# Kernel optimization log

Measured on AMD Instinct MI355X. Metric: run time of the kernel, lower is better.

Reference implementation:

```python
import jax, jax.numpy as jnp
import numpy as np

EPS = 1e-10

def setup_inputs() -> dict:
    key = jax.random.key(0)
    k1, k2, k3 = jax.random.split(key, 3)
    B, K, M, X, Y = 64, 4, 3, 256, 256
    predictions = jax.random.uniform(k1, (B, K, X, Y), dtype=jnp.float32)
    inputs = jax.random.normal(k2, (B, M, X, Y), dtype=jnp.float32)
    heart = jax.random.randint(k3, (B, 1, X, Y), 0, 2, dtype=jnp.int32)
    return {"predictions": predictions, "inputs": inputs, "heart": heart}

def reference(predictions, inputs, heart):
    B, K, X, Y = predictions.shape
    M = inputs.shape[1]
    P = X * Y
    pred = predictions.reshape(B, K, P)            # [B,K,P]
    inp = inputs.reshape(B, M, P)                  # [B,M,P]
    w = (heart.reshape(B, P) == 1).astype(pred.dtype)  # ROI mask [B,P]
    pw = pred * w[:, None, :]                      # masked responsibilities [B,K,P]
    s = pw.sum(-1) + EPS                           # [B,K]
    # weighted means/vars over masked pixels
    mu = jnp.einsum('bkp,bmp->bkm', pw, inp) / s[..., None]        # [B,K,M]
    diff = inp[:, None, :, :] - mu[..., None]                      # [B,K,M,P]
    var = jnp.einsum('bkmp,bkp->bkm', diff * diff, pw) / s[..., None] + EPS
    # per-channel Gaussian pdf, product over channels M
    pdf = jnp.exp(-diff * diff / (2.0 * var[..., None])) / jnp.sqrt(2.0 * jnp.pi * var)[..., None]
    temp = jnp.prod(pdf, axis=2)                   # [B,K,P]
    mix = jnp.sum(pred * temp, axis=1)             # [B,P]
    ll = jnp.log(mix + EPS)
    n = w.sum(-1)                                   # pixels in ROI per sample
    loss_b = -(ll * w).sum(-1) / n                 # mean over masked pixels
    return jnp.mean(loss_b)
```

## Files before the change

### kernel.cpp

```cpp
#include <hip/hip_runtime.h>

#define EPS 1e-10f

constexpr int B_ = 64, K_ = 4, M_ = 3, P_ = 65536;
constexpr int THREADS = 256;
constexpr int CHUNK = 2048;
constexpr int BLOCKS_PER_B = P_ / CHUNK;
constexpr int VPT = CHUNK / 4 / THREADS;
constexpr int WAVE_ITERS = CHUNK / 4 / 64;
constexpr int NACC = 29;

__global__ __launch_bounds__(THREADS, 4) void gmm_pass1(
    const float* __restrict__ pred, const float* __restrict__ inp,
    const int* __restrict__ heart, float* __restrict__ sums)
{
    const int blk   = blockIdx.x;
    const int b     = blk / BLOCKS_PER_B;
    const int chunk = blk % BLOCKS_PER_B;
    const int tid   = threadIdx.x;
    const int wv    = tid >> 6;
    const int lane  = tid & 63;

    const float4* pkb = (const float4*)(pred + ((size_t)b * K_ + wv) * P_);
    const float4* ib  = (const float4*)(inp  + (size_t)b * M_ * P_);
    const int4*   hb  = (const int4*)(heart + (size_t)b * P_);
    const int vbase = chunk * (CHUNK / 4);

    float s = 0.f, n = 0.f;
    float t0 = 0.f, t1 = 0.f, t2 = 0.f;
    float u0 = 0.f, u1 = 0.f, u2 = 0.f;

    int v = vbase + lane;
    float4 p_c  = pkb[v];
    float4 x0_c = ib[0 * (P_ / 4) + v];
    float4 x1_c = ib[1 * (P_ / 4) + v];
    float4 x2_c = ib[2 * (P_ / 4) + v];
    int4   h_c  = hb[v];

    #pragma unroll
    for (int it = 0; it < WAVE_ITERS; ++it) {
        float4 p_n, x0_n, x1_n, x2_n; int4 h_n;
        if (it + 1 < WAVE_ITERS) {
            const int vn = vbase + (it + 1) * 64 + lane;
            p_n  = pkb[vn];
            x0_n = ib[0 * (P_ / 4) + vn];
            x1_n = ib[1 * (P_ / 4) + vn];
            x2_n = ib[2 * (P_ / 4) + vn];
            h_n  = hb[vn];
        }

        #define PIX1(C) do {                                                  \
            const float w  = (h_c.C == 1) ? 1.f : 0.f;                        \
            const float pw = p_c.C * w;                                       \
            n += w; s += pw;                                                  \
            t0 = fmaf(pw, x0_c.C, t0);                                        \
            u0 = fmaf(pw * x0_c.C, x0_c.C, u0);                               \
            t1 = fmaf(pw, x1_c.C, t1);                                        \
            u1 = fmaf(pw * x1_c.C, x1_c.C, u1);                               \
            t2 = fmaf(pw, x2_c.C, t2);                                        \
            u2 = fmaf(pw * x2_c.C, x2_c.C, u2);                               \
        } while (0)
        PIX1(x); PIX1(y); PIX1(z); PIX1(w);
        #undef PIX1

        if (it + 1 < WAVE_ITERS) {
            p_c = p_n; x0_c = x0_n; x1_c = x1_n; x2_c = x2_n; h_c = h_n;
        }
    }

    float vals[8] = { s, t0, t1, t2, u0, u1, u2, n };
    __shared__ float lds[4 * 8];
    #pragma unroll
    for (int j = 0; j < 8; ++j) {
        float x = vals[j];
        #pragma unroll
        for (int off = 32; off; off >>= 1) x += __shfl_down(x, off);
        vals[j] = x;
    }
    if (lane == 0) {
        #pragma unroll
        for (int j = 0; j < 8; ++j) lds[wv * 8 + j] = vals[j];
    }
    __syncthreads();
    if (tid < 32) {
        const int w = tid >> 3, j = tid & 7;
        int idx;
        bool emit = true;
        if (j == 0)      idx = w;
        else if (j <= 3) idx = 4  + w * 3 + (j - 1);
        else if (j <= 6) idx = 16 + w * 3 + (j - 4);
        else { idx = 28; emit = (w == 0); }
        if (emit) atomicAdd(&sums[b * NACC + idx], lds[tid]);
    }
}

__global__ void gmm_pass2(const float* __restrict__ sums, float* __restrict__ der)
{
    const int t = blockIdx.x * blockDim.x + threadIdx.x;
    if (t >= B_ * K_) return;
    const int b = t / K_, k = t % K_;
    const float* sb = sums + b * NACC;
    float* db = der + b * NACC;

    const float s = sb[k] + EPS;
    const float inv_s = 1.f / s;
    float c = 1.f;
    #pragma unroll
    for (int m = 0; m < M_; ++m) {
        const float tkm = sb[4  + k * M_ + m];
        const float ukm = sb[16 + k * M_ + m];
        const float mu  = tkm * inv_s;
        const float var = fmaf(-mu, mu, ukm * inv_s) + EPS;
        db[k * M_ + m]      = mu;
        db[12 + k * M_ + m] = 0.5f / var;
        c *= rsqrtf(6.283185307179586f * var);
    }
    db[24 + k] = c;
    if (k == 0) db[28] = 1.f / (sb[28] * (float)B_);
}

__global__ __launch_bounds__(THREADS, 4) void gmm_pass3(
    const float* __restrict__ pred, const float* __restrict__ inp,
    const int* __restrict__ heart, const float* __restrict__ der,
    float* __restrict__ out)
{
    const int blk   = blockIdx.x;
    const int b     = blk / BLOCKS_PER_B;
    const int chunk = blk % BLOCKS_PER_B;
    const int tid   = threadIdx.x;

    const float* db = der + b * NACC;
    float mu[K_][M_], iv[K_][M_], ck[K_];
    #pragma unroll
    for (int k = 0; k < K_; ++k) {
        #pragma unroll
        for (int m = 0; m < M_; ++m) {
            mu[k][m] = db[k * M_ + m];
            iv[k][m] = db[12 + k * M_ + m];
        }
        ck[k] = db[24 + k];
    }
    const float invn = db[28];

    const float4* pb = (const float4*)(pred + (size_t)b * K_ * P_);
    const float4* ib = (const float4*)(inp  + (size_t)b * M_ * P_);
    const int4*   hb = (const int4*)(heart + (size_t)b * P_);
    const int vbase = chunk * (CHUNK / 4);

    float part = 0.f;
    #pragma unroll
    for (int it = 0; it < VPT; ++it) {
        const int v = vbase + it * THREADS + tid;
        const int4 h4 = hb[v];
        float4 pk[K_];
        float4 xm[M_];
        #pragma unroll
        for (int k = 0; k < K_; ++k) pk[k] = pb[k * (P_ / 4) + v];
        #pragma unroll
        for (int m = 0; m < M_; ++m) xm[m] = ib[m * (P_ / 4) + v];

        #define PIX3(C) do {                                                  \
            const float w = (h4.C == 1) ? 1.f : 0.f;                          \
            float mix = EPS;                                                  \
            _Pragma("unroll")                                                 \
            for (int k = 0; k < K_; ++k) {                                    \
                float e = 0.f;                                                \
                _Pragma("unroll")                                             \
                for (int m = 0; m < M_; ++m) {                                \
                    const float d = xm[m].C - mu[k][m];                       \
                    e = fmaf(-(d * d), iv[k][m], e);                          \
                }                                                             \
                mix = fmaf(pk[k].C * ck[k], __expf(e), mix);                  \
            }                                                                 \
            part = fmaf(w, __logf(mix), part);                                \
        } while (0)
        PIX3(x); PIX3(y); PIX3(z); PIX3(w);
        #undef PIX3
    }

    __shared__ float lds[4];
    const int lane = tid & 63, wid = tid >> 6;
    float v = part;
    #pragma unroll
    for (int off = 32; off; off >>= 1) v += __shfl_down(v, off);
    if (lane == 0) lds[wid] = v;
    __syncthreads();
    if (tid == 0) {
        const float s = lds[0] + lds[1] + lds[2] + lds[3];
        atomicAdd(out, -s * invn);
    }
}

extern "C" void kernel_launch(void* const* d_in, const int* in_sizes, int n_in,
                              void* d_out, int out_size, void* d_ws, size_t ws_size,
                              hipStream_t stream)
{
    const float* pred  = (const float*)d_in[0];
    const float* inp   = (const float*)d_in[1];
    const int*   heart = (const int*)d_in[2];
    float* out = (float*)d_out;
    float* ws  = (float*)d_ws;

    float* sums = ws;
    float* der  = ws + B_ * NACC;

    hipMemsetAsync(sums, 0, B_ * NACC * sizeof(float), stream);
    hipMemsetAsync(out,  0, sizeof(float), stream);

    gmm_pass1<<<B_ * BLOCKS_PER_B, THREADS, 0, stream>>>(pred, inp, heart, sums);
    gmm_pass2<<<1, 256, 0, stream>>>(sums, der);
    gmm_pass3<<<B_ * BLOCKS_PER_B, THREADS, 0, stream>>>(pred, inp, heart, der, out);
}
```

Baseline: 69.11 us.

## Stage inputs through LDS with double-buffered async global_load_lds in both passes

Both streaming passes now copy each 512-pixel tile of all eight planes (4 pred, 3 inp, heart) into a double-buffered LDS array with global_load_lds, prefetching the next tile while computing the current one. Chunk size per block is doubled, halving the grid. The aim is to keep more memory traffic in flight and decouple loads from the register pipeline. In exchange it adds 32KB of LDS per block, a barrier per tile and lower pass3 occupancy, and there is no explicit vmcnt wait before the barrier, so correctness depends on how the compiler orders the async copy.

```diff
diff --git a/kernel.cpp b/kernel.cpp
--- a/kernel.cpp
+++ b/kernel.cpp
@@ -4,68 +4,75 @@
 
 constexpr int B_ = 64, K_ = 4, M_ = 3, P_ = 65536;
 constexpr int THREADS = 256;
-constexpr int CHUNK = 2048;
+constexpr int CHUNK = 4096;
 constexpr int BLOCKS_PER_B = P_ / CHUNK;
-constexpr int VPT = CHUNK / 4 / THREADS;
-constexpr int WAVE_ITERS = CHUNK / 4 / 64;
+constexpr int TILE = 512;
+constexpr int NT = CHUNK / TILE;
+constexpr int NPL = 8;
 constexpr int NACC = 29;
+
+__device__ __forceinline__ void stage_tile(
+    const float* __restrict__ pred, const float* __restrict__ inp,
+    const int* __restrict__ heart, int b, int pix0,
+    float (*sbuf)[NPL][TILE], int buf, int wv, int lane)
+{
+    #pragma unroll
+    for (int j = 0; j < 4; ++j) {
+        const int r  = wv * 4 + j;
+        const int pl = r >> 1;
+        const int hf = r & 1;
+        const float* g;
+        if (pl < 4)       g = pred + ((size_t)(b * K_ + pl)) * P_ + pix0 + hf * 256;
+        else if (pl < 7)  g = inp  + ((size_t)(b * M_ + (pl - 4))) * P_ + pix0 + hf * 256;
+        else              g = (const float*)(heart + (size_t)b * P_ + pix0 + hf * 256);
+        __builtin_amdgcn_global_load_lds(g + lane * 4, &sbuf[buf][pl][hf * 256], 16, 0, 0);
+    }
+}
 
 __global__ __launch_bounds__(THREADS, 4) void gmm_pass1(
     const float* __restrict__ pred, const float* __restrict__ inp,
     const int* __restrict__ heart, float* __restrict__ sums)
 {
+    __shared__ float sbuf[2][NPL][TILE];
     const int blk   = blockIdx.x;
     const int b     = blk / BLOCKS_PER_B;
     const int chunk = blk % BLOCKS_PER_B;
     const int tid   = threadIdx.x;
     const int wv    = tid >> 6;
     const int lane  = tid & 63;
-
-    const float4* pkb = (const float4*)(pred + ((size_t)b * K_ + wv) * P_);
-    const float4* ib  = (const float4*)(inp  + (size_t)b * M_ * P_);
-    const int4*   hb  = (const int4*)(heart + (size_t)b * P_);
-    const int vbase = chunk * (CHUNK / 4);
+    const int base  = chunk * CHUNK;
 
     float s = 0.f, n = 0.f;
     float t0 = 0.f, t1 = 0.f, t2 = 0.f;
     float u0 = 0.f, u1 = 0.f, u2 = 0.f;
 
-    int v = vbase + lane;
-    float4 p_c  = pkb[v];
-    float4 x0_c = ib[0 * (P_ / 4) + v];
-    float4 x1_c = ib[1 * (P_ / 4) + v];
-    float4 x2_c = ib[2 * (P_ / 4) + v];
-    int4   h_c  = hb[v];
-
-    #pragma unroll
-    for (int it = 0; it < WAVE_ITERS; ++it) {
-        float4 p_n, x0_n, x1_n, x2_n; int4 h_n;
-        if (it + 1 < WAVE_ITERS) {
-            const int vn = vbase + (it + 1) * 64 + lane;
-            p_n  = pkb[vn];
-            x0_n = ib[0 * (P_ / 4) + vn];
-            x1_n = ib[1 * (P_ / 4) + vn];
-            x2_n = ib[2 * (P_ / 4) + vn];
-            h_n  = hb[vn];
+    stage_tile(pred, inp, heart, b, base, sbuf, 0, wv, lane);
+    __syncthreads();
+
+    for (int t = 0; t < NT; ++t) {
+        const int cur = t & 1;
+        if (t + 1 < NT)
+            stage_tile(pred, inp, heart, b, base + (t + 1) * TILE, sbuf, cur ^ 1, wv, lane);
+        __builtin_amdgcn_sched_barrier(0);
+
+        const float* pk  = &sbuf[cur][wv][0];
+        const float* x0p = &sbuf[cur][4][0];
+        const float* x1p = &sbuf[cur][5][0];
+        const float* x2p = &sbuf[cur][6][0];
+        const int*   hp  = (const int*)&sbuf[cur][7][0];
+
+        #pragma unroll
+        for (int g = 0; g < TILE / 64; ++g) {
+            const int px = g * 64 + lane;
+            const float w  = (hp[px] == 1) ? 1.f : 0.f;
+            const float pw = pk[px] * w;
+            n += w; s += pw;
+            float x;
+            x = x0p[px]; t0 = fmaf(pw, x, t0); u0 = fmaf(pw * x, x, u0);
+            x = x1p[px]; t1 = fmaf(pw, x, t1); u1 = fmaf(pw * x, x, u1);
+            x = x2p[px]; t2 = fmaf(pw, x, t2); u2 = fmaf(pw * x, x, u2);
         }
-
-        #define PIX1(C) do {                                                  \
-            const float w  = (h_c.C == 1) ? 1.f : 0.f;                        \
-            const float pw = p_c.C * w;                                       \
-            n += w; s += pw;                                                  \
-            t0 = fmaf(pw, x0_c.C, t0);                                        \
-            u0 = fmaf(pw * x0_c.C, x0_c.C, u0);                               \
-            t1 = fmaf(pw, x1_c.C, t1);                                        \
-            u1 = fmaf(pw * x1_c.C, x1_c.C, u1);                               \
-            t2 = fmaf(pw, x2_c.C, t2);                                        \
-            u2 = fmaf(pw * x2_c.C, x2_c.C, u2);                               \
-        } while (0)
-        PIX1(x); PIX1(y); PIX1(z); PIX1(w);
-        #undef PIX1
-
-        if (it + 1 < WAVE_ITERS) {
-            p_c = p_n; x0_c = x0_n; x1_c = x1_n; x2_c = x2_n; h_c = h_n;
-        }
+        __syncthreads();
     }
 
     float vals[8] = { s, t0, t1, t2, u0, u1, u2, n };
@@ -119,15 +126,19 @@
     if (k == 0) db[28] = 1.f / (sb[28] * (float)B_);
 }
 
-__global__ __launch_bounds__(THREADS, 4) void gmm_pass3(
+__global__ __launch_bounds__(THREADS, 3) void gmm_pass3(
     const float* __restrict__ pred, const float* __restrict__ inp,
     const int* __restrict__ heart, const float* __restrict__ der,
     float* __restrict__ out)
 {
+    __shared__ float sbuf[2][NPL][TILE];
     const int blk   = blockIdx.x;
     const int b     = blk / BLOCKS_PER_B;
     const int chunk = blk % BLOCKS_PER_B;
     const int tid   = threadIdx.x;
+    const int wv    = tid >> 6;
+    const int lane  = tid & 63;
+    const int base  = chunk * CHUNK;
 
     const float* db = der + b * NACC;
     float mu[K_][M_], iv[K_][M_], ck[K_];
@@ -142,52 +153,50 @@
     }
     const float invn = db[28];
 
-    const float4* pb = (const float4*)(pred + (size_t)b * K_ * P_);
-    const float4* ib = (const float4*)(inp  + (size_t)b * M_ * P_);
-    const int4*   hb = (const int4*)(heart + (size_t)b * P_);
-    const int vbase = chunk * (CHUNK / 4);
-
     float part = 0.f;
-    #pragma unroll
-    for (int it = 0; it < VPT; ++it) {
-        const int v = vbase + it * THREADS + tid;
-        const int4 h4 = hb[v];
-        float4 pk[K_];
-        float4 xm[M_];
-        #pragma unroll
-        for (int k = 0; k < K_; ++k) pk[k] = pb[k * (P_ / 4) + v];
-        #pragma unroll
-        for (int m = 0; m < M_; ++m) xm[m] = ib[m * (P_ / 4) + v];
-
-        #define PIX3(C) do {                                                  \
-            const float w = (h4.C == 1) ? 1.f : 0.f;                          \
-            float mix = EPS;                                                  \
-            _Pragma("unroll")                                                 \
-            for (int k = 0; k < K_; ++k) {                                    \
-                float e = 0.f;                                                \
-                _Pragma("unroll")                                             \
-                for (int m = 0; m < M_; ++m) {                                \
-                    const float d = xm[m].C - mu[k][m];                       \
-                    e = fmaf(-(d * d), iv[k][m], e);                          \
-                }                                                             \
-                mix = fmaf(pk[k].C * ck[k], __expf(e), mix);                  \
-            }                                                                 \
-            part = fmaf(w, __logf(mix), part);                                \
-        } while (0)
-        PIX3(x); PIX3(y); PIX3(z); PIX3(w);
-        #undef PIX3
+
+    stage_tile(pred, inp, heart, b, base, sbuf, 0, wv, lane);
+    __syncthreads();
+
+    for (int t = 0; t < NT; ++t) {
+        const int cur = t & 1;
+        if (t + 1 < NT)
+            stage_tile(pred, inp, heart, b, base + (t + 1) * TILE, sbuf, cur ^ 1, wv, lane);
+        __builtin_amdgcn_sched_barrier(0);
+
+        const int* hp = (const int*)&sbuf[cur][7][0];
+        #pragma unroll
+        for (int i = 0; i < TILE / THREADS; ++i) {
+            const int px = i * THREADS + tid;
+            const float w = (hp[px] == 1) ? 1.f : 0.f;
+            const float x0 = sbuf[cur][4][px];
+            const float x1 = sbuf[cur][5][px];
+            const float x2 = sbuf[cur][6][px];
+            float mix = EPS;
+            #pragma unroll
+            for (int k = 0; k < K_; ++k) {
+                const float d0 = x0 - mu[k][0];
+                const float d1 = x1 - mu[k][1];
+                const float d2 = x2 - mu[k][2];
+                float e = -(d0 * d0) * iv[k][0];
+                e = fmaf(-(d1 * d1), iv[k][1], e);
+                e = fmaf(-(d2 * d2), iv[k][2], e);
+                mix = fmaf(sbuf[cur][k][px] * ck[k], __expf(e), mix);
+            }
+            part = fmaf(w, __logf(mix), part);
+        }
+        __syncthreads();
     }
 
     __shared__ float lds[4];
-    const int lane = tid & 63, wid = tid >> 6;
     float v = part;
     #pragma unroll
     for (int off = 32; off; off >>= 1) v += __shfl_down(v, off);
-    if (lane == 0) lds[wid] = v;
+    if (lane == 0) lds[wv] = v;
     __syncthreads();
     if (tid == 0) {
-        const float s = lds[0] + lds[1] + lds[2] + lds[3];
-        atomicAdd(out, -s * invn);
+        const float ssum = lds[0] + lds[1] + lds[2] + lds[3];
+        atomicAdd(out, -ssum * invn);
     }
 }
 
```

After: 67.13 us. -2.9%, faster.
